# Kernel tuning notes

Measured on AMD Instinct MI355X. Metric: run time of the kernel, lower is better.

The kernel has to match this reference:

```python
import jax, jax.numpy as jnp
import numpy as np

B, S, D, F, E, TOP_K = 4, 1024, 512, 2048, 16, 2
TEMPERATURE = 0.5
STD = 0.02


def setup_inputs() -> dict:
    key = jax.random.key(0)
    ks = jax.random.split(key, 9)
    f32 = jnp.float32
    return {
        "x": jax.random.normal(ks[0], (B, S, D), f32),
        # router gate: Linear(D, D//2) -> ReLU -> Linear(D//2, E)
        "gate_w1": jax.random.normal(ks[1], (D, D // 2), f32) * STD,
        "gate_b1": jnp.zeros((D // 2,), f32),
        "gate_w2": jax.random.normal(ks[2], (D // 2, E), f32) * STD,
        "gate_b2": jnp.zeros((E,), f32),
        # stacked expert weights (E experts, each D->F->D)
        "up_w": jax.random.normal(ks[3], (E, D, F), f32) * STD,
        "up_b": jnp.zeros((E, F), f32),
        "down_w": jax.random.normal(ks[4], (E, F, D), f32) * STD,
        "down_b": jnp.zeros((E, D), f32),
    }


def reference(x, gate_w1, gate_b1, gate_w2, gate_b2, up_w, up_b, down_w, down_b):
    num_experts = up_w.shape[0]
    # ---- router ----
    h = jax.nn.relu(x @ gate_w1 + gate_b1)                      # [B,S,D//2]
    scores = h @ gate_w2 + gate_b2                              # [B,S,E]
    routing_probs = jax.nn.softmax(scores / TEMPERATURE, axis=-1)
    # load-balance loss: MSE(mean usage, uniform)
    batch_usage = routing_probs.mean(axis=(0, 1))               # [E]
    load_balance_loss = jnp.mean((batch_usage - 1.0 / num_experts) ** 2)
    # ---- top-k routing weights, renormalized via softmax over selected scores ----
    top_vals, top_idx = jax.lax.top_k(routing_probs, TOP_K)     # [B,S,K]
    top_probs = jax.nn.softmax(top_vals, axis=-1)               # [B,S,K]
    # scatter per-token top-k probs into dense [B,S,E] combine weights
    expert_probs = jnp.einsum(
        "bske,bsk->bse", jax.nn.one_hot(top_idx, num_experts, dtype=x.dtype), top_probs
    )
    # ---- every expert computed densely on all tokens, masked combine (faithful to source) ----
    hid = jax.nn.gelu(
        jnp.einsum("bsd,edf->ebsf", x, up_w) + up_b[:, None, None, :],
        approximate=False,
    )                                                            # [E,B,S,F]
    expert_out = jnp.einsum("ebsf,efd->ebsd", hid, down_w) + down_b[:, None, None, :]
    output = jnp.einsum("ebsd,bse->bsd", expert_out, expert_probs)  # [B,S,D]
    return output, load_balance_loss, routing_probs
```

## Files before the change

kernel.cpp:

```cpp
#include <hip/hip_runtime.h>
#include <hip/hip_bf16.h>

#define NTOK 4096
#define DIM  512
#define DH   256
#define NE   16
#define FF   2048
#define CAP  8192
#define MAXTILES 80
#define TEMP_INV 2.0f
#define RTOK 8

#define OUT_LOSS  (NTOK * DIM)
#define OUT_PROBS (NTOK * DIM + 1)

#define WS_CNT    0
#define WS_USAGE  64
#define WS_NTILES 128
#define WS_DESC   256
#define WS_WTS    1024
#define WS_LISTS  36864
#define WS_HID    (1u << 20)
#define WS_PAIR   (48u << 20)

typedef __attribute__((ext_vector_type(8))) short bf16x8;
typedef __attribute__((ext_vector_type(8))) unsigned short u16x8;
typedef __attribute__((ext_vector_type(4))) float f32x4;

__device__ __forceinline__ unsigned short f2bf(float f) {
  union { float f; unsigned u; } c; c.f = f;
  return (unsigned short)((c.u + 0x7FFFu + ((c.u >> 16) & 1u)) >> 16);
}
__device__ __forceinline__ float gc(const float4& v, int c) {
  return c == 0 ? v.x : c == 1 ? v.y : c == 2 ? v.z : v.w;
}

__launch_bounds__(256)
__global__ void router_kernel(const float* __restrict__ x,
                              const float* __restrict__ w1,
                              const float* __restrict__ b1,
                              const float* __restrict__ w2,
                              const float* __restrict__ b2,
                              float* __restrict__ out,
                              int* __restrict__ cnt,
                              float* __restrict__ usage,
                              float* __restrict__ wts,
                              int* __restrict__ lists) {
  __shared__ __align__(16) float xs[RTOK][DIM];
  __shared__ __align__(16) float hs[RTOK][DH + 4];
  __shared__ __align__(16) float w2s[DH * NE];
  __shared__ float ps[RTOK][NE];
  __shared__ float us[2][NE];

  int tid = threadIdx.x;
  int tok0 = blockIdx.x * RTOK;

  {
    const float4* xg = (const float4*)(x + (size_t)tok0 * DIM);
    float4* xv = (float4*)&xs[0][0];
    for (int i = tid; i < RTOK * DIM / 4; i += 256) xv[i] = xg[i];
    for (int i = tid; i < DH * NE; i += 256) w2s[i] = w2[i];
  }
  __syncthreads();

  {
    int j = tid;
    float acc[RTOK];
    float bj = b1[j];
#pragma unroll
    for (int t = 0; t < RTOK; ++t) acc[t] = bj;

    float wq[4][4];
#pragma unroll
    for (int g = 0; g < 4; ++g)
#pragma unroll
      for (int u = 0; u < 4; ++u)
        wq[g][u] = w1[(size_t)(g * 4 + u) * DH + j];

#pragma unroll 4
    for (int g = 0; g < DIM / 4; ++g) {
      float wcur[4];
#pragma unroll
      for (int u = 0; u < 4; ++u) wcur[u] = wq[g & 3][u];
      int gn = g + 4;
      if (gn < DIM / 4) {
#pragma unroll
        for (int u = 0; u < 4; ++u) wq[g & 3][u] = w1[(size_t)(gn * 4 + u) * DH + j];
      }
      int k = g * 4;
#pragma unroll
      for (int t = 0; t < RTOK; ++t) {
        float4 xq = *(const float4*)&xs[t][k];
        acc[t] = fmaf(xq.x, wcur[0], acc[t]);
        acc[t] = fmaf(xq.y, wcur[1], acc[t]);
        acc[t] = fmaf(xq.z, wcur[2], acc[t]);
        acc[t] = fmaf(xq.w, wcur[3], acc[t]);
      }
    }
#pragma unroll
    for (int t = 0; t < RTOK; ++t) hs[t][j] = fmaxf(acc[t], 0.f);
  }
  __syncthreads();

  int t = tid >> 4, e = tid & 15;
  if (tid < 128) {
    float s = b2[e];
#pragma unroll 8
    for (int jj = 0; jj < DH; ++jj) s = fmaf(hs[t][jj], w2s[jj * NE + e], s);
    s *= TEMP_INV;
    float m = s;
#pragma unroll
    for (int d = 1; d < 16; d <<= 1) m = fmaxf(m, __shfl_xor(m, d));
    float p = expf(s - m);
    float sum = p;
#pragma unroll
    for (int d = 1; d < 16; d <<= 1) sum += __shfl_xor(sum, d);
    float prob = p / sum;
    out[OUT_PROBS + (size_t)(tok0 + t) * NE + e] = prob;
    ps[t][e] = prob;

    float v = prob;
    v += __shfl_xor(v, 16);
    v += __shfl_xor(v, 32);
    if ((tid & 63) < 16) us[tid >> 6][e] = v;
  }
  __syncthreads();
  if (tid < 16) atomicAdd(&usage[tid], us[0][tid] + us[1][tid]);

  if (tid < RTOK) {
    int tt = tid;
    float v1 = -1.f; int i1 = 0;
    for (int ee = 0; ee < NE; ++ee) { float pv = ps[tt][ee]; if (pv > v1) { v1 = pv; i1 = ee; } }
    float v2 = -1.f; int i2 = 0;
    for (int ee = 0; ee < NE; ++ee) { if (ee == i1) continue; float pv = ps[tt][ee]; if (pv > v2) { v2 = pv; i2 = ee; } }
    float mm = fmaxf(v1, v2);
    float e0 = expf(v1 - mm), e1 = expf(v2 - mm);
    float rs = 1.f / (e0 + e1);
    int gt = tok0 + tt;
    wts[2 * gt]     = e0 * rs;
    wts[2 * gt + 1] = e1 * rs;
    int p1 = atomicAdd(&cnt[i1], 1);
    lists[i1 * CAP + p1] = 2 * gt;
    int p2 = atomicAdd(&cnt[i2], 1);
    lists[i2 * CAP + p2] = 2 * gt + 1;
  }
}

__global__ void sched_kernel(const int* __restrict__ cnt,
                             const float* __restrict__ usage,
                             int* __restrict__ ntiles,
                             int2* __restrict__ desc,
                             float* __restrict__ out_loss) {
  int lane = threadIdx.x;
  int e = lane & 15;
  int c = (lane < 16) ? cnt[e] : 0;
  int tl = (c + 127) >> 7;
  int v = tl;
#pragma unroll
  for (int d = 1; d < 16; d <<= 1) {
    int u = __shfl_up(v, d);
    if (lane >= d) v += u;
  }
  int excl = v - tl;
  int tot = __shfl(v, 15);
  if (lane == 0) *ntiles = tot;
  if (lane < 16) {
    for (int i = 0; i < tl; ++i) desc[excl + i] = make_int2(e, i << 7);
    float d0 = usage[e] * (1.f / 4096.f) - (1.f / 16.f);
    float ls = d0 * d0;
#pragma unroll
    for (int d = 1; d < 16; d <<= 1) ls += __shfl_xor(ls, d);
    if (lane == 0) *out_loss = ls * (1.f / 16.f);
  }
}

__launch_bounds__(256)
__global__ void up_kernel(const float* __restrict__ x,
                          const float* __restrict__ up_w,
                          const float* __restrict__ up_b,
                          const int* __restrict__ cnt,
                          const int* __restrict__ ntiles,
                          const int2* __restrict__ desc,
                          const int* __restrict__ lists,
                          unsigned short* __restrict__ hid) {
  int ty = blockIdx.y;
  if (ty >= *ntiles) return;
  int2 dd = desc[ty];
  int e = dd.x, i0 = dd.y;
  int cntE = cnt[e];
  int f0 = blockIdx.x * 128;
  const float* __restrict__ W = up_w + (size_t)e * (DIM * FF);

  __shared__ __align__(16) unsigned short As[128 * 64];
  __shared__ __align__(16) unsigned short Bs[128 * 64];

  int tid = threadIdx.x;
  int ar = tid >> 1, ah = tid & 1;
  int aidx = i0 + ar;
  int aslot = (aidx < cntE) ? lists[e * CAP + aidx] : 0;
  const float* __restrict__ xrow = x + (size_t)(aslot >> 1) * DIM;

  int kk8 = tid >> 5;
  int n4 = (tid & 31) << 2;

  int lane = tid & 63, wid = tid >> 6;
  int wr = wid >> 1, wc = wid & 1;
  int ln15 = lane & 15, lq = lane >> 4;

  f32x4 acc[4][4];
#pragma unroll
  for (int i = 0; i < 4; ++i)
#pragma unroll
    for (int j = 0; j < 4; ++j) acc[i][j] = f32x4{0.f, 0.f, 0.f, 0.f};

  for (int ks = 0; ks < DIM / 64; ++ks) {
    int k0 = ks * 64;
#pragma unroll
    for (int i = 0; i < 4; ++i) {
      int g = (ah << 2) + i;
      float4 u = *(const float4*)(xrow + k0 + g * 8);
      float4 w = *(const float4*)(xrow + k0 + g * 8 + 4);
      u16x8 pk;
      pk[0] = f2bf(u.x); pk[1] = f2bf(u.y); pk[2] = f2bf(u.z); pk[3] = f2bf(u.w);
      pk[4] = f2bf(w.x); pk[5] = f2bf(w.y); pk[6] = f2bf(w.z); pk[7] = f2bf(w.w);
      *(u16x8*)(As + ar * 64 + ((g ^ (ar & 7)) << 3)) = pk;
    }
    float4 bw[8];
#pragma unroll
    for (int rr = 0; rr < 8; ++rr)
      bw[rr] = *(const float4*)(W + (size_t)(k0 + kk8 * 8 + rr) * FF + f0 + n4);
#pragma unroll
    for (int c = 0; c < 4; ++c) {
      int n = n4 + c;
      u16x8 pk;
#pragma unroll
      for (int rr = 0; rr < 8; ++rr) pk[rr] = f2bf(gc(bw[rr], c));
      *(u16x8*)(Bs + n * 64 + ((kk8 ^ (n & 7)) << 3)) = pk;
    }
    __syncthreads();
#pragma unroll
    for (int ksub = 0; ksub < 2; ++ksub) {
      bf16x8 a[4], b[4];
      int g = (ksub << 2) + lq;
#pragma unroll
      for (int mi = 0; mi < 4; ++mi) {
        int arow = (wr << 6) + (mi << 4) + ln15;
        a[mi] = *(const bf16x8*)(As + arow * 64 + ((g ^ (arow & 7)) << 3));
      }
#pragma unroll
      for (int ni = 0; ni < 4; ++ni) {
        int bcol = (wc << 6) + (ni << 4) + ln15;
        b[ni] = *(const bf16x8*)(Bs + bcol * 64 + ((g ^ (bcol & 7)) << 3));
      }
#pragma unroll
      for (int mi = 0; mi < 4; ++mi)
#pragma unroll
        for (int ni = 0; ni < 4; ++ni)
          acc[mi][ni] = __builtin_amdgcn_mfma_f32_16x16x32_bf16(a[mi], b[ni], acc[mi][ni], 0, 0, 0);
    }
    __syncthreads();
  }
#pragma unroll
  for (int mi = 0; mi < 4; ++mi) {
    int row_l = (wr << 6) + (mi << 4) + (lq << 2);
#pragma unroll
    for (int ni = 0; ni < 4; ++ni) {
      int col = (wc << 6) + (ni << 4) + ln15;
      float bias = up_b[e * FF + f0 + col];
#pragma unroll
      for (int q = 0; q < 4; ++q) {
        float vv = acc[mi][ni][q] + bias;
        float g = 0.5f * vv * (1.f + erff(vv * 0.70710678118f));
        hid[((size_t)ty * 128 + row_l + q) * FF + f0 + col] = f2bf(g);
      }
    }
  }
}

__launch_bounds__(256)
__global__ void down_kernel(const unsigned short* __restrict__ hid,
                            const float* __restrict__ down_w,
                            const float* __restrict__ down_b,
                            const int* __restrict__ cnt,
                            const int* __restrict__ ntiles,
                            const int2* __restrict__ desc,
                            const int* __restrict__ lists,
                            float* __restrict__ pairbuf) {
  int ty = blockIdx.y;
  if (ty >= *ntiles) return;
  int2 dd = desc[ty];
  int e = dd.x, i0 = dd.y;
  int cntE = cnt[e];
  int n0 = blockIdx.x * 128;
  const float* __restrict__ W = down_w + (size_t)e * (FF * DIM);

  __shared__ __align__(16) unsigned short As[128 * 64];
  __shared__ __align__(16) unsigned short Bs[128 * 64];

  int tid = threadIdx.x;
  int ar = tid >> 1, ah = tid & 1;
  const unsigned short* __restrict__ hrow = hid + ((size_t)ty * 128 + ar) * FF;

  int kk8 = tid >> 5;
  int n4 = (tid & 31) << 2;

  int lane = tid & 63, wid = tid >> 6;
  int wr = wid >> 1, wc = wid & 1;
  int ln15 = lane & 15, lq = lane >> 4;

  f32x4 acc[4][4];
#pragma unroll
  for (int i = 0; i < 4; ++i)
#pragma unroll
    for (int j = 0; j < 4; ++j) acc[i][j] = f32x4{0.f, 0.f, 0.f, 0.f};

  for (int ks = 0; ks < FF / 64; ++ks) {
    int k0 = ks * 64;
#pragma unroll
    for (int i = 0; i < 4; ++i) {
      int g = (ah << 2) + i;
      u16x8 pk = *(const u16x8*)(hrow + k0 + g * 8);
      *(u16x8*)(As + ar * 64 + ((g ^ (ar & 7)) << 3)) = pk;
    }
    float4 bw[8];
#pragma unroll
    for (int rr = 0; rr < 8; ++rr)
      bw[rr] = *(const float4*)(W + (size_t)(k0 + kk8 * 8 + rr) * DIM + n0 + n4);
#pragma unroll
    for (int c = 0; c < 4; ++c) {
      int n = n4 + c;
      u16x8 pk;
#pragma unroll
      for (int rr = 0; rr < 8; ++rr) pk[rr] = f2bf(gc(bw[rr], c));
      *(u16x8*)(Bs + n * 64 + ((kk8 ^ (n & 7)) << 3)) = pk;
    }
    __syncthreads();
#pragma unroll
    for (int ksub = 0; ksub < 2; ++ksub) {
      bf16x8 a[4], b[4];
      int g = (ksub << 2) + lq;
#pragma unroll
      for (int mi = 0; mi < 4; ++mi) {
        int arow = (wr << 6) + (mi << 4) + ln15;
        a[mi] = *(const bf16x8*)(As + arow * 64 + ((g ^ (arow & 7)) << 3));
      }
#pragma unroll
      for (int ni = 0; ni < 4; ++ni) {
        int bcol = (wc << 6) + (ni << 4) + ln15;
        b[ni] = *(const bf16x8*)(Bs + bcol * 64 + ((g ^ (bcol & 7)) << 3));
      }
#pragma unroll
      for (int mi = 0; mi < 4; ++mi)
#pragma unroll
        for (int ni = 0; ni < 4; ++ni)
          acc[mi][ni] = __builtin_amdgcn_mfma_f32_16x16x32_bf16(a[mi], b[ni], acc[mi][ni], 0, 0, 0);
    }
    __syncthreads();
  }
#pragma unroll
  for (int mi = 0; mi < 4; ++mi) {
    int row_l = (wr << 6) + (mi << 4) + (lq << 2);
#pragma unroll
    for (int ni = 0; ni < 4; ++ni) {
      int col = n0 + (wc << 6) + (ni << 4) + ln15;
      float bias = down_b[e * DIM + col];
#pragma unroll
      for (int q = 0; q < 4; ++q) {
        int idx = i0 + row_l + q;
        if (idx < cntE) {
          int slot = lists[e * CAP + idx];
          pairbuf[(size_t)slot * DIM + col] = acc[mi][ni][q] + bias;
        }
      }
    }
  }
}

__launch_bounds__(256)
__global__ void combine_kernel(const float* __restrict__ pairbuf,
                               const float* __restrict__ wts,
                               float* __restrict__ out) {
  int t = blockIdx.x;
  int d = threadIdx.x << 1;
  float w0 = wts[2 * t], w1 = wts[2 * t + 1];
  float2 a = *(const float2*)(pairbuf + (size_t)(2 * t) * DIM + d);
  float2 b = *(const float2*)(pairbuf + (size_t)(2 * t + 1) * DIM + d);
  float2 r; r.x = w0 * a.x + w1 * b.x; r.y = w0 * a.y + w1 * b.y;
  *(float2*)(out + (size_t)t * DIM + d) = r;
}

extern "C" void kernel_launch(void* const* d_in, const int* in_sizes, int n_in,
                              void* d_out, int out_size, void* d_ws, size_t ws_size,
                              hipStream_t stream) {
  (void)in_sizes; (void)n_in; (void)out_size; (void)ws_size;
  const float* x   = (const float*)d_in[0];
  const float* gw1 = (const float*)d_in[1];
  const float* gb1 = (const float*)d_in[2];
  const float* gw2 = (const float*)d_in[3];
  const float* gb2 = (const float*)d_in[4];
  const float* uw  = (const float*)d_in[5];
  const float* ub  = (const float*)d_in[6];
  const float* dw  = (const float*)d_in[7];
  const float* db  = (const float*)d_in[8];
  float* out = (float*)d_out;
  char* ws = (char*)d_ws;

  int*   cnt     = (int*)(ws + WS_CNT);
  float* usage   = (float*)(ws + WS_USAGE);
  int*   ntiles  = (int*)(ws + WS_NTILES);
  int2*  desc    = (int2*)(ws + WS_DESC);
  float* wts     = (float*)(ws + WS_WTS);
  int*   lists   = (int*)(ws + WS_LISTS);
  unsigned short* hid = (unsigned short*)(ws + WS_HID);
  float* pairbuf = (float*)(ws + WS_PAIR);

  hipMemsetAsync(d_ws, 0, 1024, stream);
  router_kernel<<<NTOK / RTOK, 256, 0, stream>>>(x, gw1, gb1, gw2, gb2, out, cnt, usage, wts, lists);
  sched_kernel<<<1, 64, 0, stream>>>(cnt, usage, ntiles, desc, out + OUT_LOSS);
  up_kernel<<<dim3(FF / 128, MAXTILES), 256, 0, stream>>>(x, uw, ub, cnt, ntiles, desc, lists, hid);
  down_kernel<<<dim3(DIM / 128, MAXTILES), 256, 0, stream>>>(hid, dw, db, cnt, ntiles, desc, lists, pairbuf);
  combine_kernel<<<NTOK, 256, 0, stream>>>(pairbuf, wts, out);
}
```

Measured before the change: 415.3 us.

## Pre-convert expert weights to bf16 tiles and double-buffer GEMMs with direct LDS loads

```diff
diff --git a/kernel.cpp b/kernel.cpp
--- a/kernel.cpp
+++ b/kernel.cpp
@@ -9,7 +9,6 @@
 #define CAP  8192
 #define MAXTILES 80
 #define TEMP_INV 2.0f
-#define RTOK 8
 
 #define OUT_LOSS  (NTOK * DIM)
 #define OUT_PROBS (NTOK * DIM + 1)
@@ -20,8 +19,12 @@
 #define WS_DESC   256
 #define WS_WTS    1024
 #define WS_LISTS  36864
-#define WS_HID    (1u << 20)
-#define WS_PAIR   (48u << 20)
+#define WS_H      (1ull<<20)
+#define WS_G      (1ull<<20)
+#define WS_TUP    (16ull<<20)
+#define WS_PAIR   (16ull<<20)
+#define WS_TDN    (48ull<<20)
+#define WS_HID    (80ull<<20)
 
 typedef __attribute__((ext_vector_type(8))) short bf16x8;
 typedef __attribute__((ext_vector_type(8))) unsigned short u16x8;
@@ -31,103 +34,167 @@
   union { float f; unsigned u; } c; c.f = f;
   return (unsigned short)((c.u + 0x7FFFu + ((c.u >> 16) & 1u)) >> 16);
 }
-__device__ __forceinline__ float gc(const float4& v, int c) {
-  return c == 0 ? v.x : c == 1 ? v.y : c == 2 ? v.z : v.w;
-}
+
+#define GLOAD16(gp, lp) __builtin_amdgcn_global_load_lds( \
+    (const __attribute__((address_space(1))) void*)(gp), \
+    (__attribute__((address_space(3))) void*)(lp), 16, 0, 0)
 
 __launch_bounds__(256)
-__global__ void router_kernel(const float* __restrict__ x,
+__global__ void fused0_kernel(const float* __restrict__ x,
                               const float* __restrict__ w1,
                               const float* __restrict__ b1,
-                              const float* __restrict__ w2,
-                              const float* __restrict__ b2,
-                              float* __restrict__ out,
-                              int* __restrict__ cnt,
-                              float* __restrict__ usage,
-                              float* __restrict__ wts,
-                              int* __restrict__ lists) {
-  __shared__ __align__(16) float xs[RTOK][DIM];
-  __shared__ __align__(16) float hs[RTOK][DH + 4];
-  __shared__ __align__(16) float w2s[DH * NE];
-  __shared__ float ps[RTOK][NE];
-  __shared__ float us[2][NE];
-
+                              const float* __restrict__ up_w,
+                              const float* __restrict__ down_w,
+                              float* __restrict__ H,
+                              unsigned short* __restrict__ Tup,
+                              unsigned short* __restrict__ Tdn) {
+  __shared__ __align__(16) char smem[33792];
+  int bx = blockIdx.x, tid = threadIdx.x;
+
+  if (bx < 512) {
+    float* As = (float*)smem;
+    float* Bs = (float*)(smem + 32 * 68 * 4);
+    int mb = bx >> 3, nb = bx & 7;
+    int tok0 = mb * 64, n0 = nb * 32;
+    int ty = tid >> 4, tx = tid & 15;
+    float acc[4][2];
+#pragma unroll
+    for (int i = 0; i < 4; ++i) { acc[i][0] = 0.f; acc[i][1] = 0.f; }
+
+    for (int kc = 0; kc < 16; ++kc) {
+      int k0 = kc * 32;
+      {
+        int tk = tid >> 2, kg = (tid & 3) * 8;
+        const float* xp = x + (size_t)(tok0 + tk) * DIM + k0 + kg;
+        float4 v0 = *(const float4*)xp;
+        float4 v1 = *(const float4*)(xp + 4);
+        As[(kg + 0) * 68 + tk] = v0.x; As[(kg + 1) * 68 + tk] = v0.y;
+        As[(kg + 2) * 68 + tk] = v0.z; As[(kg + 3) * 68 + tk] = v0.w;
+        As[(kg + 4) * 68 + tk] = v1.x; As[(kg + 5) * 68 + tk] = v1.y;
+        As[(kg + 6) * 68 + tk] = v1.z; As[(kg + 7) * 68 + tk] = v1.w;
+      }
+      {
+        int k = tid >> 3, nn = (tid & 7) * 4;
+        *(float4*)&Bs[k * 36 + nn] = *(const float4*)(w1 + (size_t)(k0 + k) * DH + n0 + nn);
+      }
+      __syncthreads();
+#pragma unroll 8
+      for (int k = 0; k < 32; ++k) {
+        float4 a = *(const float4*)&As[k * 68 + ty * 4];
+        float2 b = *(const float2*)&Bs[k * 36 + tx * 2];
+#pragma unroll
+        for (int i = 0; i < 4; ++i) {
+          float av = (i == 0) ? a.x : (i == 1) ? a.y : (i == 2) ? a.z : a.w;
+          acc[i][0] = fmaf(av, b.x, acc[i][0]);
+          acc[i][1] = fmaf(av, b.y, acc[i][1]);
+        }
+      }
+      __syncthreads();
+    }
+    float bj0 = b1[n0 + tx * 2], bj1 = b1[n0 + tx * 2 + 1];
+#pragma unroll
+    for (int i = 0; i < 4; ++i) {
+      float2 st;
+      st.x = fmaxf(acc[i][0] + bj0, 0.f);
+      st.y = fmaxf(acc[i][1] + bj1, 0.f);
+      *(float2*)(H + (size_t)(tok0 + ty * 4 + i) * DH + n0 + tx * 2) = st;
+    }
+  } else {
+    const float* src; unsigned short* dst; int srcStride;
+    if (bx < 1536) {
+      int u = bx - 512;
+      int e = u >> 6, kc = (u >> 3) & 7, fb = u & 7;
+      src = up_w + (size_t)e * DIM * FF + (size_t)kc * 64 * FF + fb * 256;
+      srcStride = FF;
+      dst = Tup + ((size_t)(e * 8 + kc) * FF + fb * 256) * 64;
+    } else {
+      int d = bx - 1536;
+      int e = d >> 6, kc = (d >> 1) & 31, nb = d & 1;
+      src = down_w + (size_t)e * FF * DIM + (size_t)kc * 64 * DIM + nb * 256;
+      srcStride = DIM;
+      dst = Tdn + ((size_t)(e * 32 + kc) * DIM + nb * 256) * 64;
+    }
+    unsigned short* L = (unsigned short*)smem;
+#pragma unroll
+    for (int i = 0; i < 16; ++i) {
+      int idx = tid + i * 256;
+      int row = idx >> 6, c4 = idx & 63;
+      float4 v = *(const float4*)(src + (size_t)row * srcStride + c4 * 4);
+      unsigned short* p = L + row * 264 + c4 * 4;
+      p[0] = f2bf(v.x); p[1] = f2bf(v.y); p[2] = f2bf(v.z); p[3] = f2bf(v.w);
+    }
+    __syncthreads();
+#pragma unroll
+    for (int j = 0; j < 8; ++j) {
+      u16x8 pk;
+#pragma unroll
+      for (int k = 0; k < 8; ++k) pk[k] = L[(j * 8 + k) * 264 + tid];
+      *(u16x8*)(dst + (size_t)tid * 64 + j * 8) = pk;
+    }
+  }
+}
+
+__launch_bounds__(256)
+__global__ void score_kernel(const float* __restrict__ H,
+                             const float* __restrict__ w2,
+                             const float* __restrict__ b2,
+                             float* __restrict__ out,
+                             int* __restrict__ cnt,
+                             float* __restrict__ usage,
+                             float* __restrict__ wts,
+                             int* __restrict__ lists) {
+  __shared__ __align__(16) float hs[16][260];
+  __shared__ __align__(16) float w2t[16][260];
+  __shared__ float ps[16][NE];
+  __shared__ float us[4][NE];
   int tid = threadIdx.x;
-  int tok0 = blockIdx.x * RTOK;
-
+  int tok0 = blockIdx.x * 16;
   {
-    const float4* xg = (const float4*)(x + (size_t)tok0 * DIM);
-    float4* xv = (float4*)&xs[0][0];
-    for (int i = tid; i < RTOK * DIM / 4; i += 256) xv[i] = xg[i];
-    for (int i = tid; i < DH * NE; i += 256) w2s[i] = w2[i];
+    int r = tid >> 4, seg = tid & 15;
+    const float* hp = H + (size_t)(tok0 + r) * DH + seg * 16;
+    *(float4*)&hs[r][seg * 16 + 0]  = *(const float4*)(hp + 0);
+    *(float4*)&hs[r][seg * 16 + 4]  = *(const float4*)(hp + 4);
+    *(float4*)&hs[r][seg * 16 + 8]  = *(const float4*)(hp + 8);
+    *(float4*)&hs[r][seg * 16 + 12] = *(const float4*)(hp + 12);
+  }
+  {
+    float4 a = *(const float4*)(w2 + (size_t)tid * 16 + 0);
+    float4 b = *(const float4*)(w2 + (size_t)tid * 16 + 4);
+    float4 c = *(const float4*)(w2 + (size_t)tid * 16 + 8);
+    float4 d = *(const float4*)(w2 + (size_t)tid * 16 + 12);
+    w2t[0][tid] = a.x;  w2t[1][tid] = a.y;  w2t[2][tid] = a.z;  w2t[3][tid] = a.w;
+    w2t[4][tid] = b.x;  w2t[5][tid] = b.y;  w2t[6][tid] = b.z;  w2t[7][tid] = b.w;
+    w2t[8][tid] = c.x;  w2t[9][tid] = c.y;  w2t[10][tid] = c.z; w2t[11][tid] = c.w;
+    w2t[12][tid] = d.x; w2t[13][tid] = d.y; w2t[14][tid] = d.z; w2t[15][tid] = d.w;
   }
   __syncthreads();
-
-  {
-    int j = tid;
-    float acc[RTOK];
-    float bj = b1[j];
-#pragma unroll
-    for (int t = 0; t < RTOK; ++t) acc[t] = bj;
-
-    float wq[4][4];
-#pragma unroll
-    for (int g = 0; g < 4; ++g)
-#pragma unroll
-      for (int u = 0; u < 4; ++u)
-        wq[g][u] = w1[(size_t)(g * 4 + u) * DH + j];
-
+  int t = tid >> 4, e = tid & 15;
+  float s = b2[e];
 #pragma unroll 4
-    for (int g = 0; g < DIM / 4; ++g) {
-      float wcur[4];
-#pragma unroll
-      for (int u = 0; u < 4; ++u) wcur[u] = wq[g & 3][u];
-      int gn = g + 4;
-      if (gn < DIM / 4) {
-#pragma unroll
-        for (int u = 0; u < 4; ++u) wq[g & 3][u] = w1[(size_t)(gn * 4 + u) * DH + j];
-      }
-      int k = g * 4;
-#pragma unroll
-      for (int t = 0; t < RTOK; ++t) {
-        float4 xq = *(const float4*)&xs[t][k];
-        acc[t] = fmaf(xq.x, wcur[0], acc[t]);
-        acc[t] = fmaf(xq.y, wcur[1], acc[t]);
-        acc[t] = fmaf(xq.z, wcur[2], acc[t]);
-        acc[t] = fmaf(xq.w, wcur[3], acc[t]);
-      }
-    }
-#pragma unroll
-    for (int t = 0; t < RTOK; ++t) hs[t][j] = fmaxf(acc[t], 0.f);
-  }
+  for (int j4 = 0; j4 < 64; ++j4) {
+    float4 hv = *(const float4*)&hs[t][j4 * 4];
+    float4 wv = *(const float4*)&w2t[e][j4 * 4];
+    s = fmaf(hv.x, wv.x, fmaf(hv.y, wv.y, fmaf(hv.z, wv.z, fmaf(hv.w, wv.w, s))));
+  }
+  s *= TEMP_INV;
+  float m = s;
+#pragma unroll
+  for (int d = 1; d < 16; d <<= 1) m = fmaxf(m, __shfl_xor(m, d));
+  float p = expf(s - m);
+  float sum = p;
+#pragma unroll
+  for (int d = 1; d < 16; d <<= 1) sum += __shfl_xor(sum, d);
+  float prob = p / sum;
+  out[OUT_PROBS + (size_t)(tok0 + t) * NE + e] = prob;
+  ps[t][e] = prob;
+  float v = prob;
+  v += __shfl_xor(v, 16);
+  v += __shfl_xor(v, 32);
+  if ((tid & 63) < 16) us[tid >> 6][e] = v;
   __syncthreads();
-
-  int t = tid >> 4, e = tid & 15;
-  if (tid < 128) {
-    float s = b2[e];
-#pragma unroll 8
-    for (int jj = 0; jj < DH; ++jj) s = fmaf(hs[t][jj], w2s[jj * NE + e], s);
-    s *= TEMP_INV;
-    float m = s;
-#pragma unroll
-    for (int d = 1; d < 16; d <<= 1) m = fmaxf(m, __shfl_xor(m, d));
-    float p = expf(s - m);
-    float sum = p;
-#pragma unroll
-    for (int d = 1; d < 16; d <<= 1) sum += __shfl_xor(sum, d);
-    float prob = p / sum;
-    out[OUT_PROBS + (size_t)(tok0 + t) * NE + e] = prob;
-    ps[t][e] = prob;
-
-    float v = prob;
-    v += __shfl_xor(v, 16);
-    v += __shfl_xor(v, 32);
-    if ((tid & 63) < 16) us[tid >> 6][e] = v;
-  }
-  __syncthreads();
-  if (tid < 16) atomicAdd(&usage[tid], us[0][tid] + us[1][tid]);
-
-  if (tid < RTOK) {
+  if (tid < 16) atomicAdd(&usage[tid], us[0][tid] + us[1][tid] + us[2][tid] + us[3][tid]);
+
+  if (tid < 16) {
     int tt = tid;
     float v1 = -1.f; int i1 = 0;
     for (int ee = 0; ee < NE; ++ee) { float pv = ps[tt][ee]; if (pv > v1) { v1 = pv; i1 = ee; } }
@@ -175,111 +242,128 @@
 }
 
 __launch_bounds__(256)
-__global__ void up_kernel(const float* __restrict__ x,
-                          const float* __restrict__ up_w,
-                          const float* __restrict__ up_b,
-                          const int* __restrict__ cnt,
-                          const int* __restrict__ ntiles,
-                          const int2* __restrict__ desc,
-                          const int* __restrict__ lists,
-                          unsigned short* __restrict__ hid) {
-  int ty = blockIdx.y;
+__global__ void gather_kernel(const float* __restrict__ x,
+                              const int* __restrict__ cnt,
+                              const int* __restrict__ ntiles,
+                              const int2* __restrict__ desc,
+                              const int* __restrict__ lists,
+                              unsigned short* __restrict__ G) {
+  int ty = blockIdx.x;
   if (ty >= *ntiles) return;
   int2 dd = desc[ty];
   int e = dd.x, i0 = dd.y;
   int cntE = cnt[e];
+  int tid = threadIdx.x, r = tid >> 1, h = tid & 1;
+  int aidx = i0 + r;
+  bool valid = aidx < cntE;
+  int slot = valid ? lists[e * CAP + aidx] : 0;
+  const float* xrow = x + (size_t)(slot >> 1) * DIM;
+  unsigned short* gb = G + (size_t)ty * 65536;
+#pragma unroll
+  for (int c4 = 0; c4 < 4; ++c4) {
+    int chunk = h * 4 + c4;
+    unsigned short* dst = gb + (size_t)chunk * 8192 + r * 64;
+#pragma unroll
+    for (int j = 0; j < 8; ++j) {
+      u16x8 pk;
+      if (valid) {
+        float4 u = *(const float4*)(xrow + chunk * 64 + j * 8);
+        float4 w = *(const float4*)(xrow + chunk * 64 + j * 8 + 4);
+        pk[0] = f2bf(u.x); pk[1] = f2bf(u.y); pk[2] = f2bf(u.z); pk[3] = f2bf(u.w);
+        pk[4] = f2bf(w.x); pk[5] = f2bf(w.y); pk[6] = f2bf(w.z); pk[7] = f2bf(w.w);
+      } else {
+        pk = u16x8{0, 0, 0, 0, 0, 0, 0, 0};
+      }
+      *(u16x8*)(dst + j * 8) = pk;
+    }
+  }
+}
+
+__launch_bounds__(256)
+__global__ void up_kernel(const unsigned short* __restrict__ G,
+                          const unsigned short* __restrict__ Tup,
+                          const float* __restrict__ up_b,
+                          const int* __restrict__ ntiles,
+                          const int2* __restrict__ desc,
+                          unsigned short* __restrict__ hid) {
+  int ty = blockIdx.y;
+  if (ty >= *ntiles) return;
+  int e = desc[ty].x;
   int f0 = blockIdx.x * 128;
-  const float* __restrict__ W = up_w + (size_t)e * (DIM * FF);
-
-  __shared__ __align__(16) unsigned short As[128 * 64];
-  __shared__ __align__(16) unsigned short Bs[128 * 64];
-
-  int tid = threadIdx.x;
-  int ar = tid >> 1, ah = tid & 1;
-  int aidx = i0 + ar;
-  int aslot = (aidx < cntE) ? lists[e * CAP + aidx] : 0;
-  const float* __restrict__ xrow = x + (size_t)(aslot >> 1) * DIM;
-
-  int kk8 = tid >> 5;
-  int n4 = (tid & 31) << 2;
-
-  int lane = tid & 63, wid = tid >> 6;
-  int wr = wid >> 1, wc = wid & 1;
-  int ln15 = lane & 15, lq = lane >> 4;
-
+  __shared__ __align__(16) unsigned short Ab[2][128 * 64];
+  __shared__ __align__(16) unsigned short Bb[2][128 * 64];
+  int tid = threadIdx.x, lane = tid & 63, wid = tid >> 6;
+  const unsigned short* Asrc = G + (size_t)ty * 65536;
+  const unsigned short* Bsrc = Tup + ((size_t)(e * 8) * FF + f0) * 64;
+
+  int wr = wid >> 1, wc = wid & 1, ln15 = lane & 15, lq = lane >> 4;
   f32x4 acc[4][4];
 #pragma unroll
   for (int i = 0; i < 4; ++i)
 #pragma unroll
     for (int j = 0; j < 4; ++j) acc[i][j] = f32x4{0.f, 0.f, 0.f, 0.f};
 
-  for (int ks = 0; ks < DIM / 64; ++ks) {
-    int k0 = ks * 64;
-#pragma unroll
-    for (int i = 0; i < 4; ++i) {
-      int g = (ah << 2) + i;
-      float4 u = *(const float4*)(xrow + k0 + g * 8);
-      float4 w = *(const float4*)(xrow + k0 + g * 8 + 4);
-      u16x8 pk;
-      pk[0] = f2bf(u.x); pk[1] = f2bf(u.y); pk[2] = f2bf(u.z); pk[3] = f2bf(u.w);
-      pk[4] = f2bf(w.x); pk[5] = f2bf(w.y); pk[6] = f2bf(w.z); pk[7] = f2bf(w.w);
-      *(u16x8*)(As + ar * 64 + ((g ^ (ar & 7)) << 3)) = pk;
-    }
-    float4 bw[8];
-#pragma unroll
-    for (int rr = 0; rr < 8; ++rr)
-      bw[rr] = *(const float4*)(W + (size_t)(k0 + kk8 * 8 + rr) * FF + f0 + n4);
-#pragma unroll
-    for (int c = 0; c < 4; ++c) {
-      int n = n4 + c;
-      u16x8 pk;
-#pragma unroll
-      for (int rr = 0; rr < 8; ++rr) pk[rr] = f2bf(gc(bw[rr], c));
-      *(u16x8*)(Bs + n * 64 + ((kk8 ^ (n & 7)) << 3)) = pk;
-    }
-    __syncthreads();
+#define UP_STAGE(b, kc) do {                                          \
+    const unsigned short* a_ = Asrc + (size_t)(kc) * 8192;            \
+    const unsigned short* b_ = Bsrc + (size_t)(kc) * FF * 64;         \
+    _Pragma("unroll")                                                 \
+    for (int i_ = 0; i_ < 4; ++i_) {                                  \
+      int off_ = (wid * 4 + i_) * 512;                                \
+      GLOAD16(a_ + off_ + lane * 8, &Ab[b][off_]);                    \
+      GLOAD16(b_ + off_ + lane * 8, &Bb[b][off_]);                    \
+    }                                                                 \
+  } while (0)
+
+  UP_STAGE(0, 0);
+  asm volatile("s_waitcnt vmcnt(0)" ::: "memory");
+  __syncthreads();
+  int cur = 0;
+  for (int kc = 0; kc < 8; ++kc) {
+    if (kc < 7) UP_STAGE(cur ^ 1, kc + 1);
+    const unsigned short* As = Ab[cur];
+    const unsigned short* Bs = Bb[cur];
 #pragma unroll
     for (int ksub = 0; ksub < 2; ++ksub) {
       bf16x8 a[4], b[4];
       int g = (ksub << 2) + lq;
 #pragma unroll
-      for (int mi = 0; mi < 4; ++mi) {
-        int arow = (wr << 6) + (mi << 4) + ln15;
-        a[mi] = *(const bf16x8*)(As + arow * 64 + ((g ^ (arow & 7)) << 3));
-      }
-#pragma unroll
-      for (int ni = 0; ni < 4; ++ni) {
-        int bcol = (wc << 6) + (ni << 4) + ln15;
-        b[ni] = *(const bf16x8*)(Bs + bcol * 64 + ((g ^ (bcol & 7)) << 3));
-      }
+      for (int mi = 0; mi < 4; ++mi)
+        a[mi] = *(const bf16x8*)(As + ((wr << 6) + (mi << 4) + ln15) * 64 + (g << 3));
+#pragma unroll
+      for (int ni = 0; ni < 4; ++ni)
+        b[ni] = *(const bf16x8*)(Bs + ((wc << 6) + (ni << 4) + ln15) * 64 + (g << 3));
 #pragma unroll
       for (int mi = 0; mi < 4; ++mi)
 #pragma unroll
         for (int ni = 0; ni < 4; ++ni)
           acc[mi][ni] = __builtin_amdgcn_mfma_f32_16x16x32_bf16(a[mi], b[ni], acc[mi][ni], 0, 0, 0);
     }
+    asm volatile("s_waitcnt vmcnt(0)" ::: "memory");
     __syncthreads();
+    cur ^= 1;
   }
 #pragma unroll
   for (int mi = 0; mi < 4; ++mi) {
-    int row_l = (wr << 6) + (mi << 4) + (lq << 2);
+    int row = (wr << 6) + (mi << 4) + (lq << 2);
 #pragma unroll
     for (int ni = 0; ni < 4; ++ni) {
       int col = (wc << 6) + (ni << 4) + ln15;
       float bias = up_b[e * FF + f0 + col];
+      size_t base = ((size_t)(ty * 32 + (f0 >> 6) + (col >> 6)) * 128 + row) * 64 + (col & 63);
 #pragma unroll
       for (int q = 0; q < 4; ++q) {
         float vv = acc[mi][ni][q] + bias;
-        float g = 0.5f * vv * (1.f + erff(vv * 0.70710678118f));
-        hid[((size_t)ty * 128 + row_l + q) * FF + f0 + col] = f2bf(g);
+        float gl = 0.5f * vv * (1.f + erff(vv * 0.70710678118f));
+        hid[base + (size_t)q * 64] = f2bf(gl);
       }
     }
   }
+#undef UP_STAGE
 }
 
 __launch_bounds__(256)
 __global__ void down_kernel(const unsigned short* __restrict__ hid,
-                            const float* __restrict__ down_w,
+                            const unsigned short* __restrict__ Tdn,
                             const float* __restrict__ down_b,
                             const int* __restrict__ cnt,
                             const int* __restrict__ ntiles,
@@ -291,82 +375,71 @@
   int2 dd = desc[ty];
   int e = dd.x, i0 = dd.y;
   int cntE = cnt[e];
-  int n0 = blockIdx.x * 128;
-  const float* __restrict__ W = down_w + (size_t)e * (FF * DIM);
-
-  __shared__ __align__(16) unsigned short As[128 * 64];
-  __shared__ __align__(16) unsigned short Bs[128 * 64];
-
-  int tid = threadIdx.x;
-  int ar = tid >> 1, ah = tid & 1;
-  const unsigned short* __restrict__ hrow = hid + ((size_t)ty * 128 + ar) * FF;
-
-  int kk8 = tid >> 5;
-  int n4 = (tid & 31) << 2;
-
-  int lane = tid & 63, wid = tid >> 6;
-  int wr = wid >> 1, wc = wid & 1;
-  int ln15 = lane & 15, lq = lane >> 4;
-
-  f32x4 acc[4][4];
-#pragma unroll
-  for (int i = 0; i < 4; ++i)
-#pragma unroll
-    for (int j = 0; j < 4; ++j) acc[i][j] = f32x4{0.f, 0.f, 0.f, 0.f};
-
-  for (int ks = 0; ks < FF / 64; ++ks) {
-    int k0 = ks * 64;
-#pragma unroll
-    for (int i = 0; i < 4; ++i) {
-      int g = (ah << 2) + i;
-      u16x8 pk = *(const u16x8*)(hrow + k0 + g * 8);
-      *(u16x8*)(As + ar * 64 + ((g ^ (ar & 7)) << 3)) = pk;
-    }
-    float4 bw[8];
-#pragma unroll
-    for (int rr = 0; rr < 8; ++rr)
-      bw[rr] = *(const float4*)(W + (size_t)(k0 + kk8 * 8 + rr) * DIM + n0 + n4);
-#pragma unroll
-    for (int c = 0; c < 4; ++c) {
-      int n = n4 + c;
-      u16x8 pk;
-#pragma unroll
-      for (int rr = 0; rr < 8; ++rr) pk[rr] = f2bf(gc(bw[rr], c));
-      *(u16x8*)(Bs + n * 64 + ((kk8 ^ (n & 7)) << 3)) = pk;
-    }
+  int n0 = blockIdx.x * 64;
+  __shared__ __align__(16) unsigned short Ab[2][128 * 64];
+  __shared__ __align__(16) unsigned short Bb[2][64 * 64];
+  int tid = threadIdx.x, lane = tid & 63, wid = tid >> 6;
+  const unsigned short* Asrc = hid + (size_t)ty * 32 * 8192;
+  const unsigned short* Bsrc = Tdn + ((size_t)(e * 32) * DIM + n0) * 64;
+
+  int wr = wid >> 1, wc = wid & 1, ln15 = lane & 15, lq = lane >> 4;
+  f32x4 acc[4][2];
+#pragma unroll
+  for (int i = 0; i < 4; ++i) { acc[i][0] = f32x4{0.f,0.f,0.f,0.f}; acc[i][1] = f32x4{0.f,0.f,0.f,0.f}; }
+
+#define DN_STAGE(b, kc) do {                                          \
+    const unsigned short* a_ = Asrc + (size_t)(kc) * 8192;            \
+    const unsigned short* b_ = Bsrc + (size_t)(kc) * DIM * 64;        \
+    _Pragma("unroll")                                                 \
+    for (int i_ = 0; i_ < 4; ++i_) {                                  \
+      int off_ = (wid * 4 + i_) * 512;                                \
+      GLOAD16(a_ + off_ + lane * 8, &Ab[b][off_]);                    \
+    }                                                                 \
+    _Pragma("unroll")                                                 \
+    for (int i_ = 0; i_ < 2; ++i_) {                                  \
+      int off_ = (wid * 2 + i_) * 512;                                \
+      GLOAD16(b_ + off_ + lane * 8, &Bb[b][off_]);                    \
+    }                                                                 \
+  } while (0)
+
+  DN_STAGE(0, 0);
+  asm volatile("s_waitcnt vmcnt(0)" ::: "memory");
+  __syncthreads();
+  int cur = 0;
+  for (int kc = 0; kc < 32; ++kc) {
+    if (kc < 31) DN_STAGE(cur ^ 1, kc + 1);
+    const unsigned short* As = Ab[cur];
+    const unsigned short* Bs = Bb[cur];
+#pragma unroll
+    for (int ksub = 0; ksub < 2; ++ksub) {
+      bf16x8 a[4], b[2];
+      int g = (ksub << 2) + lq;
+#pragma unroll
+      for (int mi = 0; mi < 4; ++mi)
+        a[mi] = *(const bf16x8*)(As + ((wr << 6) + (mi << 4) + ln15) * 64 + (g << 3));
+#pragma unroll
+      for (int ni = 0; ni < 2; ++ni)
+        b[ni] = *(const bf16x8*)(Bs + ((wc << 5) + (ni << 4) + ln15) * 64 + (g << 3));
+#pragma unroll
+      for (int mi = 0; mi < 4; ++mi)
+#pragma unroll
+        for (int ni = 0; ni < 2; ++ni)
+          acc[mi][ni] = __builtin_amdgcn_mfma_f32_16x16x32_bf16(a[mi], b[ni], acc[mi][ni], 0, 0, 0);
+    }
+    asm volatile("s_waitcnt vmcnt(0)" ::: "memory");
     __syncthreads();
-#pragma unroll
-    for (int ksub = 0; ksub < 2; ++ksub) {
-      bf16x8 a[4], b[4];
-      int g = (ksub << 2) + lq;
-#pragma unroll
-      for (int mi = 0; mi < 4; ++mi) {
-        int arow = (wr << 6) + (mi << 4) + ln15;
-        a[mi] = *(const bf16x8*)(As + arow * 64 + ((g ^ (arow & 7)) << 3));
-      }
-#pragma unroll
-      for (int ni = 0; ni < 4; ++ni) {
-        int bcol = (wc << 6) + (ni << 4) + ln15;
-        b[ni] = *(const bf16x8*)(Bs + bcol * 64 + ((g ^ (bcol & 7)) << 3));
-      }
-#pragma unroll
-      for (int mi = 0; mi < 4; ++mi)
-#pragma unroll
-        for (int ni = 0; ni < 4; ++ni)
-          acc[mi][ni] = __builtin_amdgcn_mfma_f32_16x16x32_bf16(a[mi], b[ni], acc[mi][ni], 0, 0, 0);
-    }
-    __syncthreads();
+    cur ^= 1;
   }
 #pragma unroll
   for (int mi = 0; mi < 4; ++mi) {
-    int row_l = (wr << 6) + (mi << 4) + (lq << 2);
-#pragma unroll
-    for (int ni = 0; ni < 4; ++ni) {
-      int col = n0 + (wc << 6) + (ni << 4) + ln15;
+    int row = (wr << 6) + (mi << 4) + (lq << 2);
+#pragma unroll
+    for (int ni = 0; ni < 2; ++ni) {
+      int col = n0 + (wc << 5) + (ni << 4) + ln15;
       float bias = down_b[e * DIM + col];
 #pragma unroll
       for (int q = 0; q < 4; ++q) {
-        int idx = i0 + row_l + q;
+        int idx = i0 + row + q;
         if (idx < cntE) {
           int slot = lists[e * CAP + idx];
           pairbuf[(size_t)slot * DIM + col] = acc[mi][ni][q] + bias;
@@ -374,6 +447,7 @@
       }
     }
   }
+#undef DN_STAGE
 }
 
 __launch_bounds__(256)
@@ -411,13 +485,19 @@
   int2*  desc    = (int2*)(ws + WS_DESC);
   float* wts     = (float*)(ws + WS_WTS);
   int*   lists   = (int*)(ws + WS_LISTS);
+  float* H       = (float*)(ws + WS_H);
+  unsigned short* G   = (unsigned short*)(ws + WS_G);
+  unsigned short* Tup = (unsigned short*)(ws + WS_TUP);
+  unsigned short* Tdn = (unsigned short*)(ws + WS_TDN);
   unsigned short* hid = (unsigned short*)(ws + WS_HID);
   float* pairbuf = (float*)(ws + WS_PAIR);
 
   hipMemsetAsync(d_ws, 0, 1024, stream);
-  router_kernel<<<NTOK / RTOK, 256, 0, stream>>>(x, gw1, gb1, gw2, gb2, out, cnt, usage, wts, lists);
+  fused0_kernel<<<2560, 256, 0, stream>>>(x, gw1, gb1, uw, dw, H, Tup, Tdn);
+  score_kernel<<<NTOK / 16, 256, 0, stream>>>(H, gw2, gb2, out, cnt, usage, wts, lists);
   sched_kernel<<<1, 64, 0, stream>>>(cnt, usage, ntiles, desc, out + OUT_LOSS);
-  up_kernel<<<dim3(FF / 128, MAXTILES), 256, 0, stream>>>(x, uw, ub, cnt, ntiles, desc, lists, hid);
-  down_kernel<<<dim3(DIM / 128, MAXTILES), 256, 0, stream>>>(hid, dw, db, cnt, ntiles, desc, lists, pairbuf);
+  gather_kernel<<<MAXTILES, 256, 0, stream>>>(x, cnt, ntiles, desc, lists, G);
+  up_kernel<<<dim3(FF / 128, MAXTILES), 256, 0, stream>>>(G, Tup, ub, ntiles, desc, hid);
+  down_kernel<<<dim3(DIM / 64, MAXTILES), 256, 0, stream>>>(hid, Tdn, db, cnt, ntiles, desc, lists, pairbuf);
   combine_kernel<<<NTOK, 256, 0, stream>>>(pairbuf, wts, out);
 }
```

Result: faster. 379.0 us (-8.7%).
